# Kernel optimization log

Measured on AMD Instinct MI355X. Metric: run time of the kernel, lower is better.

The kernel has to match this reference:

```python
import jax, jax.numpy as jnp
import numpy as np

N_CHANNELS = 1024
N_HEADS = 16
BLOCK_SIZE = 2048
BATCH = 4
SEQ = 2048


def setup_inputs() -> dict:
    key = jax.random.key(0)
    k_x, k_wqkv, k_wproj = jax.random.split(key, 3)
    x = jax.random.normal(k_x, (BATCH, SEQ, N_CHANNELS), dtype=jnp.float32)
    # torch nn.Linear: y = x @ W.T + b, W shape [out, in], init normal(std=0.02)
    W_qkv = jax.random.normal(k_wqkv, (3 * N_CHANNELS, N_CHANNELS), dtype=jnp.float32) * 0.02
    b_qkv = jnp.zeros((3 * N_CHANNELS,), dtype=jnp.float32)
    W_proj = jax.random.normal(k_wproj, (N_CHANNELS, N_CHANNELS), dtype=jnp.float32) * 0.02
    b_proj = jnp.zeros((N_CHANNELS,), dtype=jnp.float32)
    return {"x": x, "W_qkv": W_qkv, "b_qkv": b_qkv, "W_proj": W_proj, "b_proj": b_proj}


def reference(x, W_qkv, b_qkv, W_proj, b_proj):
    bs, n, n_channels = x.shape
    n_heads = N_HEADS
    head_dim = n_channels // n_heads
    scale = head_dim ** (-0.5)

    qkv = x @ W_qkv.T + b_qkv                              # [b, n, 3C]
    qkv = qkv.reshape(bs, n, 3, n_heads, head_dim)
    q, k, v = qkv[:, :, 0], qkv[:, :, 1], qkv[:, :, 2]     # [b, n, h, d]

    logits = jnp.einsum('bthc,bshc->bhts', q, k) * scale   # [b, h, t, s]
    # causal mask: log(tril(ones)) = 0 below diagonal, -inf above
    causal = jnp.tril(jnp.ones((n, n), dtype=bool))
    logits = jnp.where(causal[None, None], logits, -jnp.inf)
    attn = jax.nn.softmax(logits, axis=-1)

    output = jnp.einsum('bhts,bshc->bthc', attn, v)        # [b, t, h, d]
    output = output.reshape(bs, n, n_channels)
    output = output @ W_proj.T + b_proj
    return output
```

## Files before the change

### kernel.cpp

```cpp
#include <hip/hip_runtime.h>
#include <hip/hip_bf16.h>
#include <stdint.h>

#define BATCH 4
#define SEQ   2048
#define NC    1024
#define NH    16
#define HD    64
#define NT    16

typedef __bf16 bf16x8 __attribute__((ext_vector_type(8)));
typedef __bf16 bf16x2 __attribute__((ext_vector_type(2)));
typedef float  f32x4  __attribute__((ext_vector_type(4)));
typedef float  f32x16 __attribute__((ext_vector_type(16)));

#define DEV __device__ __forceinline__

DEV unsigned short f2bf(float f) {
    union { float f; unsigned u; } v; v.f = f;
    unsigned r = (v.u + 0x7fffu + ((v.u >> 16) & 1u)) >> 16;
    return (unsigned short)r;
}

DEV float fast_exp2(float x) {
#if __has_builtin(__builtin_amdgcn_exp2f)
    return __builtin_amdgcn_exp2f(x);
#else
    return exp2f(x);
#endif
}

DEV void plane32_swap(uint32_t& a, uint32_t& b) {
#if __has_builtin(__builtin_amdgcn_permlane32_swap)
    auto r = __builtin_amdgcn_permlane32_swap(a, b, false, false);
    a = (uint32_t)r[0];
    b = (uint32_t)r[1];
#else
    uint32_t sa = __shfl_xor(a, 32), sb = __shfl_xor(b, 32);
    const bool hi = ((threadIdx.x & 63) >= 32);
    uint32_t na = hi ? sb : a;
    uint32_t nb = hi ? b : sa;
    a = na; b = nb;
#endif
}

#define GLDS16(gsrc, ldst)                                                           \
    __builtin_amdgcn_global_load_lds(                                                \
        (const __attribute__((address_space(1))) unsigned int*)(gsrc),               \
        (__attribute__((address_space(3))) unsigned int*)(ldst), 16, 0, 0)

__global__ void cvt_kernel(const float* __restrict__ in, unsigned short* __restrict__ out, int n4) {
    int i = blockIdx.x * 256 + threadIdx.x;
    if (i >= n4) return;
    float4 v = reinterpret_cast<const float4*>(in)[i];
    ushort4 o;
    o.x = f2bf(v.x); o.y = f2bf(v.y); o.z = f2bf(v.z); o.w = f2bf(v.w);
    reinterpret_cast<ushort4*>(out)[i] = o;
}

template <bool BF16_OUT>
__global__ __launch_bounds__(256, 2) void gemm_bt_kernel(
    const unsigned short* __restrict__ A,
    const unsigned short* __restrict__ W,
    const float* __restrict__ bias,
    void* __restrict__ Cout,
    int M, int N, int K, int scale_n, float scale)
{
    __shared__ __align__(16) char Alds[128 * 128];
    __shared__ __align__(16) char Blds[128 * 128];

    const int tid = threadIdx.x;
    const int w = tid >> 6, l = tid & 63, g = l >> 4, lr = l & 15;
    const int nt = N >> 7;
    const int cpx = gridDim.x >> 3;
    const int bid = (blockIdx.x & 7) * cpx + (blockIdx.x >> 3);
    const int mtile = bid / nt, ntile = bid % nt;
    const int m0 = mtile << 7, n0 = ntile << 7;
    const int wr = (w >> 1) << 6, wc = (w & 1) << 6;

    f32x4 acc[4][4] = {};

    for (int kt = 0; kt < K; kt += 64) {
        if (kt) __syncthreads();
#pragma unroll
        for (int i = 0; i < 4; ++i) {
            const int issue = (i << 2) + w;
            const int row = (issue << 3) + (l >> 3);
            const int chunk = (l & 7) ^ (row & 7);
            GLDS16((const char*)(A + (size_t)(m0 + row) * K + kt) + (chunk << 4),
                   Alds + (issue << 10));
        }
#pragma unroll
        for (int i = 0; i < 4; ++i) {
            const int issue = (i << 2) + w;
            const int row = (issue << 3) + (l >> 3);
            const int chunk = (l & 7) ^ (row & 7);
            GLDS16((const char*)(W + (size_t)(n0 + row) * K + kt) + (chunk << 4),
                   Blds + (issue << 10));
        }
        __syncthreads();

#pragma unroll
        for (int kb = 0; kb < 2; ++kb) {
            bf16x8 af[4], bfr[4];
#pragma unroll
            for (int mf = 0; mf < 4; ++mf) {
                const int row = wr + (mf << 4) + lr;
                const int chunk = ((kb << 2) + g) ^ (row & 7);
                af[mf] = *reinterpret_cast<const bf16x8*>(Alds + row * 128 + (chunk << 4));
            }
#pragma unroll
            for (int nf = 0; nf < 4; ++nf) {
                const int row = wc + (nf << 4) + lr;
                const int chunk = ((kb << 2) + g) ^ (row & 7);
                bfr[nf] = *reinterpret_cast<const bf16x8*>(Blds + row * 128 + (chunk << 4));
            }
#pragma unroll
            for (int mf = 0; mf < 4; ++mf)
#pragma unroll
                for (int nf = 0; nf < 4; ++nf)
                    acc[mf][nf] = __builtin_amdgcn_mfma_f32_16x16x32_bf16(
                        af[mf], bfr[nf], acc[mf][nf], 0, 0, 0);
        }
    }

#pragma unroll
    for (int mf = 0; mf < 4; ++mf) {
#pragma unroll
        for (int nf = 0; nf < 4; ++nf) {
            const int n = n0 + wc + (nf << 4) + lr;
            const float bscale = (n < scale_n) ? scale : 1.0f;
            const float bv = bias[n];
#pragma unroll
            for (int r = 0; r < 4; ++r) {
                const int m = m0 + wr + (mf << 4) + (g << 2) + r;
                float v2 = (acc[mf][nf][r] + bv) * bscale;
                if (BF16_OUT)
                    ((unsigned short*)Cout)[(size_t)m * N + n] = f2bf(v2);
                else
                    ((float*)Cout)[(size_t)m * N + n] = v2;
            }
        }
    }
}

__global__ __launch_bounds__(256, 4) void attn_kernel(
    const unsigned short* __restrict__ qkv,
    unsigned short* __restrict__ ctx)
{
    __shared__ __align__(16) char Klds[2][8192];
    __shared__ __align__(16) char Vt[2][8192];

    const int tid = threadIdx.x;
    const int w = tid >> 6, l = tid & 63, hi = l >> 5, lq = l & 31;
    const int bid = blockIdx.x;
    const int s = bid >> 8, u = (bid >> 6) & 3, r0 = bid & 63;
    const int v = (s & 1) ? 3 - u : u;
    const int qt = NT - 1 - (s << 2) - v;
    const int h = r0 >> 2, b = r0 & 3;
    const unsigned short* base = qkv + (size_t)b * SEQ * 3072 + h * 64;

    const int vkey0 = (tid >> 5) << 3;
    const int vd0   = (tid & 31) << 1;
    const int vcc0  = vkey0 >> 3;
    const unsigned short* vbase = base + 2048 + (size_t)vkey0 * 3072 + vd0;

    const int q0 = (qt << 7) + (w << 5);
    const int q = q0 + lq;
    const int ntiles = (qt + 1) << 1;

    bf16x8 qfr[4];
#pragma unroll
    for (int ds = 0; ds < 4; ++ds)
        qfr[ds] = *reinterpret_cast<const bf16x8*>(
            base + (size_t)q * 3072 + (ds << 4) + (hi << 3));

    f32x16 acc0 = {}, acc1 = {};
    float mrun = -INFINITY, lrun = 0.f;

    uint32_t vreg[8];

#pragma unroll
    for (int i = 0; i < 8; ++i)
        vreg[i] = *reinterpret_cast<const uint32_t*>(vbase + (size_t)i * 3072);
#pragma unroll
    for (int i = 0; i < 2; ++i) {
        const int issue = (i << 2) + w;
        const int row = (issue << 3) + (l >> 3);
        const int chunk = (l & 7) ^ (row & 7);
        GLDS16((const char*)(base + 1024 + (size_t)row * 3072) + (chunk << 4),
               Klds[0] + (issue << 10));
    }
    {
        uint4 a, bq;
        a.x = (vreg[0] & 0xffffu) | (vreg[1] << 16);
        a.y = (vreg[2] & 0xffffu) | (vreg[3] << 16);
        a.z = (vreg[4] & 0xffffu) | (vreg[5] << 16);
        a.w = (vreg[6] & 0xffffu) | (vreg[7] << 16);
        bq.x = (vreg[0] >> 16) | (vreg[1] & 0xffff0000u);
        bq.y = (vreg[2] >> 16) | (vreg[3] & 0xffff0000u);
        bq.z = (vreg[4] >> 16) | (vreg[5] & 0xffff0000u);
        bq.w = (vreg[6] >> 16) | (vreg[7] & 0xffff0000u);
        *reinterpret_cast<uint4*>(
            Vt[0] + vd0 * 128 + ((vcc0 ^ (vd0 & 7)) << 4)) = a;
        *reinterpret_cast<uint4*>(
            Vt[0] + (vd0 + 1) * 128 + ((vcc0 ^ ((vd0 + 1) & 7)) << 4)) = bq;
    }
    __syncthreads();

    for (int t = 0; t < ntiles; ++t) {
        const int cur = t & 1;
        const int kv0 = t << 6;
        const bool pf_ = (t + 1 < ntiles);

        if (pf_) {
            const int kv1 = kv0 + 64;
#pragma unroll
            for (int i = 0; i < 8; ++i)
                vreg[i] = *reinterpret_cast<const uint32_t*>(
                    vbase + (size_t)(kv1 + i) * 3072);
#pragma unroll
            for (int i = 0; i < 2; ++i) {
                const int issue = (i << 2) + w;
                const int row = (issue << 3) + (l >> 3);
                const int chunk = (l & 7) ^ (row & 7);
                GLDS16((const char*)(base + 1024 + (size_t)(kv1 + row) * 3072) + (chunk << 4),
                       Klds[cur ^ 1] + (issue << 10));
            }
        }

        if (kv0 <= q0 + 31) {
            const bool do1 = (kv0 + 32 <= q0 + 31);

            f32x16 st0 = {}, st1 = {};
            __builtin_amdgcn_s_setprio(1);
#pragma unroll
            for (int ds = 0; ds < 4; ++ds) {
                const int chunk = (((ds << 1) + hi) ^ (lq & 7)) << 4;
                bf16x8 k0 = *reinterpret_cast<const bf16x8*>(
                    Klds[cur] + lq * 128 + chunk);
                st0 = __builtin_amdgcn_mfma_f32_32x32x16_bf16(k0, qfr[ds], st0, 0, 0, 0);
            }
            if (do1) {
#pragma unroll
                for (int ds = 0; ds < 4; ++ds) {
                    const int chunk = (((ds << 1) + hi) ^ (lq & 7)) << 4;
                    bf16x8 k1 = *reinterpret_cast<const bf16x8*>(
                        Klds[cur] + (lq + 32) * 128 + chunk);
                    st1 = __builtin_amdgcn_mfma_f32_32x32x16_bf16(k1, qfr[ds], st1, 0, 0, 0);
                }
            }
            __builtin_amdgcn_s_setprio(0);

            if (kv0 + 31 > q0) {
#pragma unroll
                for (int r = 0; r < 16; ++r) {
                    const int key = kv0 + ((r & 3) + ((r >> 2) << 3) + (hi << 2));
                    if (key > q) st0[r] = -INFINITY;
                }
            }
            if (do1 && kv0 + 63 > q0) {
#pragma unroll
                for (int r = 0; r < 16; ++r) {
                    const int key = kv0 + 32 + ((r & 3) + ((r >> 2) << 3) + (hi << 2));
                    if (key > q) st1[r] = -INFINITY;
                }
            }

            float mt = st0[0];
#pragma unroll
            for (int r = 1; r < 16; ++r) mt = fmaxf(mt, st0[r]);
            if (do1) {
#pragma unroll
                for (int r = 0; r < 16; ++r) mt = fmaxf(mt, st1[r]);
            }
            mt = fmaxf(mt, __shfl_xor(mt, 32));
            if (__any(mt > mrun + 8.0f)) {
                const float mnew = fmaxf(mrun, mt);
                const float corr = fast_exp2(mrun - mnew);
                mrun = mnew;
                lrun *= corr;
#pragma unroll
                for (int r = 0; r < 16; ++r) { acc0[r] *= corr; acc1[r] *= corr; }
            }
            float rs = 0.f;
#pragma unroll
            for (int r = 0; r < 16; ++r) { st0[r] = fast_exp2(st0[r] - mrun); rs += st0[r]; }
            if (do1) {
#pragma unroll
                for (int r = 0; r < 16; ++r) { st1[r] = fast_exp2(st1[r] - mrun); rs += st1[r]; }
            }
            rs += __shfl_xor(rs, 32);
            lrun += rs;

            uint32_t pk0[8], pk1[8];
#pragma unroll
            for (int sp = 0; sp < 4; ++sp)
#pragma unroll
                for (int c = 0; c < 2; ++c) {
                    bf16x2 t0 = {(__bf16)st0[(sp << 2) + (c << 1)],
                                 (__bf16)st0[(sp << 2) + (c << 1) + 1]};
                    pk0[(sp << 1) + c] = __builtin_bit_cast(uint32_t, t0);
                }
            if (do1) {
#pragma unroll
                for (int sp = 0; sp < 4; ++sp)
#pragma unroll
                    for (int c = 0; c < 2; ++c) {
                        bf16x2 t1 = {(__bf16)st1[(sp << 2) + (c << 1)],
                                     (__bf16)st1[(sp << 2) + (c << 1) + 1]};
                        pk1[(sp << 1) + c] = __builtin_bit_cast(uint32_t, t1);
                    }
            }

            const int nkt = do1 ? 4 : 2;
            __builtin_amdgcn_s_setprio(1);
#pragma unroll
            for (int kt = 0; kt < 4; ++kt) {
                if (kt >= nkt) break;
                const int s0 = (kt & 1) << 1;
                uint32_t x0, x1, y0, y1;
                if (kt < 2) {
                    x0 = pk0[(s0 << 1) + 0]; x1 = pk0[(s0 << 1) + 1];
                    y0 = pk0[(s0 << 1) + 2]; y1 = pk0[(s0 << 1) + 3];
                } else {
                    x0 = pk1[(s0 << 1) + 0]; x1 = pk1[(s0 << 1) + 1];
                    y0 = pk1[(s0 << 1) + 2]; y1 = pk1[(s0 << 1) + 3];
                }
                plane32_swap(x0, y0);
                plane32_swap(x1, y1);
                union { uint32_t u[4]; bf16x8 v; } pf;
                pf.u[0] = x0; pf.u[1] = x1; pf.u[2] = y0; pf.u[3] = y1;

                const int cc = (kt << 1) + hi;
                const char* vt = Vt[cur];
                bf16x8 vf0 = *reinterpret_cast<const bf16x8*>(
                    vt + lq * 128 + ((cc ^ (lq & 7)) << 4));
                bf16x8 vf1 = *reinterpret_cast<const bf16x8*>(
                    vt + (lq + 32) * 128 + ((cc ^ (lq & 7)) << 4));
                acc0 = __builtin_amdgcn_mfma_f32_32x32x16_bf16(vf0, pf.v, acc0, 0, 0, 0);
                acc1 = __builtin_amdgcn_mfma_f32_32x32x16_bf16(vf1, pf.v, acc1, 0, 0, 0);
            }
            __builtin_amdgcn_s_setprio(0);
        }

        if (pf_) {
            uint4 a, bq;
            a.x = (vreg[0] & 0xffffu) | (vreg[1] << 16);
            a.y = (vreg[2] & 0xffffu) | (vreg[3] << 16);
            a.z = (vreg[4] & 0xffffu) | (vreg[5] << 16);
            a.w = (vreg[6] & 0xffffu) | (vreg[7] << 16);
            bq.x = (vreg[0] >> 16) | (vreg[1] & 0xffff0000u);
            bq.y = (vreg[2] >> 16) | (vreg[3] & 0xffff0000u);
            bq.z = (vreg[4] >> 16) | (vreg[5] & 0xffff0000u);
            bq.w = (vreg[6] >> 16) | (vreg[7] & 0xffff0000u);
            char* vt = Vt[cur ^ 1];
            *reinterpret_cast<uint4*>(
                vt + vd0 * 128 + ((vcc0 ^ (vd0 & 7)) << 4)) = a;
            *reinterpret_cast<uint4*>(
                vt + (vd0 + 1) * 128 + ((vcc0 ^ ((vd0 + 1) & 7)) << 4)) = bq;
            __syncthreads();
        }
    }

    {
        const float li = 1.0f / lrun;
        unsigned short* op = ctx + (size_t)(b * SEQ + q) * NC + h * HD;
#pragma unroll
        for (int r = 0; r < 16; ++r) {
            const int d = (r & 3) + ((r >> 2) << 3) + (hi << 2);
            op[d] = f2bf(acc0[r] * li);
            op[d + 32] = f2bf(acc1[r] * li);
        }
    }
}

extern "C" void kernel_launch(void* const* d_in, const int* in_sizes, int n_in,
                              void* d_out, int out_size, void* d_ws, size_t ws_size,
                              hipStream_t stream) {
    const float* x     = (const float*)d_in[0];
    const float* Wqkv  = (const float*)d_in[1];
    const float* bqkv  = (const float*)d_in[2];
    const float* Wproj = (const float*)d_in[3];
    const float* bproj = (const float*)d_in[4];
    float* out = (float*)d_out;

    const int M = BATCH * SEQ;
    unsigned short* ws = (unsigned short*)d_ws;
    unsigned short* xb     = ws;
    unsigned short* wqkvb  = xb + (size_t)M * NC;
    unsigned short* wprojb = wqkvb + (size_t)3 * NC * NC;
    unsigned short* qkvb   = wprojb + (size_t)NC * NC;
    unsigned short* ctxb   = qkvb + (size_t)M * 3 * NC;

    {
        int n4 = M * NC / 4;
        cvt_kernel<<<(n4 + 255) / 256, 256, 0, stream>>>(x, xb, n4);
    }
    {
        int n4 = 3 * NC * NC / 4;
        cvt_kernel<<<(n4 + 255) / 256, 256, 0, stream>>>(Wqkv, wqkvb, n4);
    }
    {
        int n4 = NC * NC / 4;
        cvt_kernel<<<(n4 + 255) / 256, 256, 0, stream>>>(Wproj, wprojb, n4);
    }

    gemm_bt_kernel<true><<<(M / 128) * (3 * NC / 128), 256, 0, stream>>>(
        xb, wqkvb, bqkv, qkvb, M, 3 * NC, NC, NC, 0.18033688011112042f);

    attn_kernel<<<NT * NH * BATCH, 256, 0, stream>>>(qkvb, ctxb);

    gemm_bt_kernel<false><<<(M / 128) * (NC / 128), 256, 0, stream>>>(
        ctxb, wprojb, bproj, out, M, NC, NC, 0, 1.0f);
}
```

Before: 160.2 us.

## Balance causal attention by pairing query tiles and splitting KV across thread groups

The attention kernel now launches 512-thread blocks made of two 256-thread groups. Each block owns a short query tile p and its mirror 15-p. Group 0 finishes tile p, then starts the first part of tile 15-p's KV range, while group 1 processes the rest of that range. The two partial softmax states (m, l, accumulators) are merged through LDS at the end, so every group runs exactly 17 KV tiles and the per-block imbalance of causal masking goes away. In exchange it adds a cross-group merge step, a larger LDS stage buffer, a 512-thread launch bound that tightens register limits, and half as many blocks. It also changes the V-tile swizzle expression.

Measured after the change: 189.3 us. +18.1%, slower.

```diff
diff --git a/kernel.cpp b/kernel.cpp
--- a/kernel.cpp
+++ b/kernel.cpp
@@ -144,30 +144,34 @@
     }
 }
 
-__global__ __launch_bounds__(256, 4) void attn_kernel(
+__global__ __launch_bounds__(512, 4) void attn_kernel(
     const unsigned short* __restrict__ qkv,
     unsigned short* __restrict__ ctx)
 {
-    __shared__ __align__(16) char Klds[2][8192];
-    __shared__ __align__(16) char Vt[2][8192];
+    __shared__ __align__(16) char Stage[2][2][2][8192];
 
     const int tid = threadIdx.x;
-    const int w = tid >> 6, l = tid & 63, hi = l >> 5, lq = l & 31;
+    const int g = tid >> 8;
+    const int tg = tid & 255;
+    const int w = tg >> 6;
+    const int l = tid & 63, hi = l >> 5, lq = l & 31;
     const int bid = blockIdx.x;
-    const int s = bid >> 8, u = (bid >> 6) & 3, r0 = bid & 63;
-    const int v = (s & 1) ? 3 - u : u;
-    const int qt = NT - 1 - (s << 2) - v;
-    const int h = r0 >> 2, b = r0 & 3;
+    const int p = bid >> 6;
+    const int hb = bid & 63;
+    const int h = hb >> 2, b = hb & 3;
+    const int P = NT - 1 - p;
     const unsigned short* base = qkv + (size_t)b * SEQ * 3072 + h * 64;
 
-    const int vkey0 = (tid >> 5) << 3;
-    const int vd0   = (tid & 31) << 1;
-    const int vcc0  = vkey0 >> 3;
+    const int switch_t = 2 * p + 2;
+    const int jB0 = 15 - 2 * p;
+
+    const int vkey0 = (tg >> 5) << 3;
+    const int vd0   = (tg & 31) << 1;
+    const int vphys = ((tg >> 5) ^ (tg & 7)) << 4;
     const unsigned short* vbase = base + 2048 + (size_t)vkey0 * 3072 + vd0;
 
-    const int q0 = (qt << 7) + (w << 5);
-    const int q = q0 + lq;
-    const int ntiles = (qt + 1) << 1;
+    int q0 = ((g == 0) ? p : P) * 128 + (w << 5);
+    int q = q0 + lq;
 
     bf16x8 qfr[4];
 #pragma unroll
@@ -177,21 +181,22 @@
 
     f32x16 acc0 = {}, acc1 = {};
     float mrun = -INFINITY, lrun = 0.f;
-
     uint32_t vreg[8];
 
-#pragma unroll
-    for (int i = 0; i < 8; ++i)
-        vreg[i] = *reinterpret_cast<const uint32_t*>(vbase + (size_t)i * 3072);
-#pragma unroll
-    for (int i = 0; i < 2; ++i) {
-        const int issue = (i << 2) + w;
-        const int row = (issue << 3) + (l >> 3);
-        const int chunk = (l & 7) ^ (row & 7);
-        GLDS16((const char*)(base + 1024 + (size_t)row * 3072) + (chunk << 4),
-               Klds[0] + (issue << 10));
-    }
     {
+        const int j0 = (g == 0) ? 0 : jB0;
+#pragma unroll
+        for (int i = 0; i < 8; ++i)
+            vreg[i] = *reinterpret_cast<const uint32_t*>(
+                vbase + (size_t)((j0 << 6) + i) * 3072);
+#pragma unroll
+        for (int i = 0; i < 2; ++i) {
+            const int issue = (i << 2) + w;
+            const int row = (issue << 3) + (l >> 3);
+            const int chunk = (l & 7) ^ (row & 7);
+            GLDS16((const char*)(base + 1024 + (size_t)((j0 << 6) + row) * 3072) + (chunk << 4),
+                   &Stage[g][0][0][0] + (issue << 10));
+        }
         uint4 a, bq;
         a.x = (vreg[0] & 0xffffu) | (vreg[1] << 16);
         a.y = (vreg[2] & 0xffffu) | (vreg[3] << 16);
@@ -201,52 +206,73 @@
         bq.y = (vreg[2] >> 16) | (vreg[3] & 0xffff0000u);
         bq.z = (vreg[4] >> 16) | (vreg[5] & 0xffff0000u);
         bq.w = (vreg[6] >> 16) | (vreg[7] & 0xffff0000u);
-        *reinterpret_cast<uint4*>(
-            Vt[0] + vd0 * 128 + ((vcc0 ^ (vd0 & 7)) << 4)) = a;
-        *reinterpret_cast<uint4*>(
-            Vt[0] + (vd0 + 1) * 128 + ((vcc0 ^ ((vd0 + 1) & 7)) << 4)) = bq;
+        char* vt = &Stage[g][0][1][0];
+        *reinterpret_cast<uint4*>(vt + vd0 * 128 + vphys) = a;
+        *reinterpret_cast<uint4*>(vt + (vd0 + 1) * 128 + vphys) = bq;
     }
     __syncthreads();
 
-    for (int t = 0; t < ntiles; ++t) {
+    for (int t = 0; t < 17; ++t) {
         const int cur = t & 1;
-        const int kv0 = t << 6;
-        const bool pf_ = (t + 1 < ntiles);
+        const int jc = (g == 0) ? ((t < switch_t) ? t : t - switch_t) : (jB0 + t);
+        const int kv0 = jc << 6;
+        const bool pf_ = (t + 1 < 17);
 
         if (pf_) {
-            const int kv1 = kv0 + 64;
+            const int jn = (g == 0) ? ((t + 1 < switch_t) ? t + 1 : t + 1 - switch_t)
+                                    : (jB0 + t + 1);
 #pragma unroll
             for (int i = 0; i < 8; ++i)
                 vreg[i] = *reinterpret_cast<const uint32_t*>(
-                    vbase + (size_t)(kv1 + i) * 3072);
+                    vbase + (size_t)((jn << 6) + i) * 3072);
 #pragma unroll
             for (int i = 0; i < 2; ++i) {
                 const int issue = (i << 2) + w;
                 const int row = (issue << 3) + (l >> 3);
                 const int chunk = (l & 7) ^ (row & 7);
-                GLDS16((const char*)(base + 1024 + (size_t)(kv1 + row) * 3072) + (chunk << 4),
-                       Klds[cur ^ 1] + (issue << 10));
-            }
+                GLDS16((const char*)(base + 1024 + (size_t)((jn << 6) + row) * 3072) + (chunk << 4),
+                       &Stage[g][cur ^ 1][0][0] + (issue << 10));
+            }
+        }
+
+        if (g == 0 && t == switch_t) {
+            const float li = 1.0f / lrun;
+            unsigned short* op = ctx + (size_t)(b * SEQ + q) * NC + h * HD;
+#pragma unroll
+            for (int r = 0; r < 16; ++r) {
+                const int d = (r & 3) + ((r >> 2) << 3) + (hi << 2);
+                op[d] = f2bf(acc0[r] * li);
+                op[d + 32] = f2bf(acc1[r] * li);
+            }
+            q0 = P * 128 + (w << 5);
+            q = q0 + lq;
+#pragma unroll
+            for (int ds = 0; ds < 4; ++ds)
+                qfr[ds] = *reinterpret_cast<const bf16x8*>(
+                    base + (size_t)q * 3072 + (ds << 4) + (hi << 3));
+#pragma unroll
+            for (int r = 0; r < 16; ++r) { acc0[r] = 0.f; acc1[r] = 0.f; }
+            mrun = -INFINITY; lrun = 0.f;
         }
 
         if (kv0 <= q0 + 31) {
             const bool do1 = (kv0 + 32 <= q0 + 31);
+            const char* Kl = &Stage[g][cur][0][0];
+            const char* Vl = &Stage[g][cur][1][0];
 
             f32x16 st0 = {}, st1 = {};
             __builtin_amdgcn_s_setprio(1);
 #pragma unroll
             for (int ds = 0; ds < 4; ++ds) {
                 const int chunk = (((ds << 1) + hi) ^ (lq & 7)) << 4;
-                bf16x8 k0 = *reinterpret_cast<const bf16x8*>(
-                    Klds[cur] + lq * 128 + chunk);
+                bf16x8 k0 = *reinterpret_cast<const bf16x8*>(Kl + lq * 128 + chunk);
                 st0 = __builtin_amdgcn_mfma_f32_32x32x16_bf16(k0, qfr[ds], st0, 0, 0, 0);
             }
             if (do1) {
 #pragma unroll
                 for (int ds = 0; ds < 4; ++ds) {
                     const int chunk = (((ds << 1) + hi) ^ (lq & 7)) << 4;
-                    bf16x8 k1 = *reinterpret_cast<const bf16x8*>(
-                        Klds[cur] + (lq + 32) * 128 + chunk);
+                    bf16x8 k1 = *reinterpret_cast<const bf16x8*>(Kl + (lq + 32) * 128 + chunk);
                     st1 = __builtin_amdgcn_mfma_f32_32x32x16_bf16(k1, qfr[ds], st1, 0, 0, 0);
                 }
             }
@@ -314,6 +340,7 @@
             }
 
             const int nkt = do1 ? 4 : 2;
+            const int fch = (lq >> 1) & 7;
             __builtin_amdgcn_s_setprio(1);
 #pragma unroll
             for (int kt = 0; kt < 4; ++kt) {
@@ -333,11 +360,10 @@
                 pf.u[0] = x0; pf.u[1] = x1; pf.u[2] = y0; pf.u[3] = y1;
 
                 const int cc = (kt << 1) + hi;
-                const char* vt = Vt[cur];
                 bf16x8 vf0 = *reinterpret_cast<const bf16x8*>(
-                    vt + lq * 128 + ((cc ^ (lq & 7)) << 4));
+                    Vl + lq * 128 + ((cc ^ fch) << 4));
                 bf16x8 vf1 = *reinterpret_cast<const bf16x8*>(
-                    vt + (lq + 32) * 128 + ((cc ^ (lq & 7)) << 4));
+                    Vl + (lq + 32) * 128 + ((cc ^ fch) << 4));
                 acc0 = __builtin_amdgcn_mfma_f32_32x32x16_bf16(vf0, pf.v, acc0, 0, 0, 0);
                 acc1 = __builtin_amdgcn_mfma_f32_32x32x16_bf16(vf1, pf.v, acc1, 0, 0, 0);
             }
@@ -354,23 +380,58 @@
             bq.y = (vreg[2] >> 16) | (vreg[3] & 0xffff0000u);
             bq.z = (vreg[4] >> 16) | (vreg[5] & 0xffff0000u);
             bq.w = (vreg[6] >> 16) | (vreg[7] & 0xffff0000u);
-            char* vt = Vt[cur ^ 1];
-            *reinterpret_cast<uint4*>(
-                vt + vd0 * 128 + ((vcc0 ^ (vd0 & 7)) << 4)) = a;
-            *reinterpret_cast<uint4*>(
-                vt + (vd0 + 1) * 128 + ((vcc0 ^ ((vd0 + 1) & 7)) << 4)) = bq;
+            char* vt = &Stage[g][cur ^ 1][1][0];
+            *reinterpret_cast<uint4*>(vt + vd0 * 128 + vphys) = a;
+            *reinterpret_cast<uint4*>(vt + (vd0 + 1) * 128 + vphys) = bq;
             __syncthreads();
         }
     }
 
-    {
-        const float li = 1.0f / lrun;
+    __syncthreads();
+    if (g == 0) {
+        float* OA = (float*)&Stage[0][0][0][0];
+        const int L = (w << 6) + l;
+        char* lb = (char*)OA + L * 128;
+#pragma unroll
+        for (int c = 0; c < 4; ++c) {
+            f32x4 t4 = {acc0[(c << 2)], acc0[(c << 2) + 1], acc0[(c << 2) + 2], acc0[(c << 2) + 3]};
+            *reinterpret_cast<f32x4*>(lb + ((c ^ (L & 7)) << 4)) = t4;
+        }
+#pragma unroll
+        for (int c = 4; c < 8; ++c) {
+            const int r0 = (c - 4) << 2;
+            f32x4 t4 = {acc1[r0], acc1[r0 + 1], acc1[r0 + 2], acc1[r0 + 3]};
+            *reinterpret_cast<f32x4*>(lb + ((c ^ (L & 7)) << 4)) = t4;
+        }
+        float* ml = (float*)&Stage[1][0][0][0];
+        if (hi == 0) {
+            ml[(((w << 5) + lq) << 1) + 0] = mrun;
+            ml[(((w << 5) + lq) << 1) + 1] = lrun;
+        }
+    }
+    __syncthreads();
+    if (g == 1) {
+        const float* OA = (const float*)&Stage[0][0][0][0];
+        const float* ml = (const float*)&Stage[1][0][0][0];
+        const int L = (w << 6) + l;
+        const char* lb = (const char*)OA + L * 128;
+        f32x4 oa[8];
+#pragma unroll
+        for (int c = 0; c < 8; ++c)
+            oa[c] = *reinterpret_cast<const f32x4*>(lb + ((c ^ (L & 7)) << 4));
+        const float mA = ml[(((w << 5) + lq) << 1) + 0];
+        const float lA = ml[(((w << 5) + lq) << 1) + 1];
+        const float m2 = fmaxf(mA, mrun);
+        float fa = fast_exp2(mA - m2);
+        float fb = fast_exp2(mrun - m2);
+        const float inv = 1.0f / (fa * lA + fb * lrun);
+        fa *= inv; fb *= inv;
         unsigned short* op = ctx + (size_t)(b * SEQ + q) * NC + h * HD;
 #pragma unroll
         for (int r = 0; r < 16; ++r) {
             const int d = (r & 3) + ((r >> 2) << 3) + (hi << 2);
-            op[d] = f2bf(acc0[r] * li);
-            op[d + 32] = f2bf(acc1[r] * li);
+            op[d]      = f2bf(fa * oa[r >> 2][r & 3]       + fb * acc0[r]);
+            op[d + 32] = f2bf(fa * oa[4 + (r >> 2)][r & 3] + fb * acc1[r]);
         }
     }
 }
@@ -409,7 +470,7 @@
     gemm_bt_kernel<true><<<(M / 128) * (3 * NC / 128), 256, 0, stream>>>(
         xb, wqkvb, bqkv, qkvb, M, 3 * NC, NC, NC, 0.18033688011112042f);
 
-    attn_kernel<<<NT * NH * BATCH, 256, 0, stream>>>(qkvb, ctxb);
+    attn_kernel<<<8 * NH * BATCH, 512, 0, stream>>>(qkvb, ctxb);
 
     gemm_bt_kernel<false><<<(M / 128) * (NC / 128), 256, 0, stream>>>(
         ctxb, wprojb, bproj, out, M, NC, NC, 0, 1.0f);
```

## Make attention kernel persistent with atomic ticket work queue over causal tiles

Applied to the files above, without the earlier changes.

Turns the attention kernel into a persistent kernel. Each block repeatedly takes a work item from a global atomic ticket, ordered longest causal query tile first, until the queue is empty. The ticket is reset by the first conversion kernel, and the grid is fixed at 1280 blocks with launch bounds raised to 5 blocks per SM. The aim is better dynamic load balancing of the uneven causal workloads, in exchange for atomic and extra barrier overhead per item and higher register pressure from the occupancy hint. The setprio hints around the MFMA sections are also removed.

After: 631.0 us. 294% more time.

```diff
diff --git a/kernel.cpp b/kernel.cpp
--- a/kernel.cpp
+++ b/kernel.cpp
@@ -8,6 +8,7 @@
 #define NH    16
 #define HD    64
 #define NT    16
+#define NITEMS (NT * NH * BATCH)
 
 typedef __bf16 bf16x8 __attribute__((ext_vector_type(8)));
 typedef __bf16 bf16x2 __attribute__((ext_vector_type(2)));
@@ -49,7 +50,9 @@
         (const __attribute__((address_space(1))) unsigned int*)(gsrc),               \
         (__attribute__((address_space(3))) unsigned int*)(ldst), 16, 0, 0)
 
-__global__ void cvt_kernel(const float* __restrict__ in, unsigned short* __restrict__ out, int n4) {
+__global__ void cvt_kernel(const float* __restrict__ in, unsigned short* __restrict__ out,
+                           int n4, unsigned int* ticket) {
+    if (ticket && blockIdx.x == 0 && threadIdx.x == 0) *ticket = 0;
     int i = blockIdx.x * 256 + threadIdx.x;
     if (i >= n4) return;
     float4 v = reinterpret_cast<const float4*>(in)[i];
@@ -144,207 +147,64 @@
     }
 }
 
-__global__ __launch_bounds__(256, 4) void attn_kernel(
+__global__ __launch_bounds__(256, 5) void attn_kernel(
     const unsigned short* __restrict__ qkv,
-    unsigned short* __restrict__ ctx)
+    unsigned short* __restrict__ ctx,
+    unsigned int* __restrict__ ticket)
 {
     __shared__ __align__(16) char Klds[2][8192];
     __shared__ __align__(16) char Vt[2][8192];
 
     const int tid = threadIdx.x;
     const int w = tid >> 6, l = tid & 63, hi = l >> 5, lq = l & 31;
-    const int bid = blockIdx.x;
-    const int s = bid >> 8, u = (bid >> 6) & 3, r0 = bid & 63;
-    const int v = (s & 1) ? 3 - u : u;
-    const int qt = NT - 1 - (s << 2) - v;
-    const int h = r0 >> 2, b = r0 & 3;
-    const unsigned short* base = qkv + (size_t)b * SEQ * 3072 + h * 64;
 
     const int vkey0 = (tid >> 5) << 3;
     const int vd0   = (tid & 31) << 1;
-    const int vcc0  = vkey0 >> 3;
-    const unsigned short* vbase = base + 2048 + (size_t)vkey0 * 3072 + vd0;
-
-    const int q0 = (qt << 7) + (w << 5);
-    const int q = q0 + lq;
-    const int ntiles = (qt + 1) << 1;
-
-    bf16x8 qfr[4];
-#pragma unroll
-    for (int ds = 0; ds < 4; ++ds)
-        qfr[ds] = *reinterpret_cast<const bf16x8*>(
-            base + (size_t)q * 3072 + (ds << 4) + (hi << 3));
-
-    f32x16 acc0 = {}, acc1 = {};
-    float mrun = -INFINITY, lrun = 0.f;
-
-    uint32_t vreg[8];
-
-#pragma unroll
-    for (int i = 0; i < 8; ++i)
-        vreg[i] = *reinterpret_cast<const uint32_t*>(vbase + (size_t)i * 3072);
-#pragma unroll
-    for (int i = 0; i < 2; ++i) {
-        const int issue = (i << 2) + w;
-        const int row = (issue << 3) + (l >> 3);
-        const int chunk = (l & 7) ^ (row & 7);
-        GLDS16((const char*)(base + 1024 + (size_t)row * 3072) + (chunk << 4),
-               Klds[0] + (issue << 10));
-    }
-    {
-        uint4 a, bq;
-        a.x = (vreg[0] & 0xffffu) | (vreg[1] << 16);
-        a.y = (vreg[2] & 0xffffu) | (vreg[3] << 16);
-        a.z = (vreg[4] & 0xffffu) | (vreg[5] << 16);
-        a.w = (vreg[6] & 0xffffu) | (vreg[7] << 16);
-        bq.x = (vreg[0] >> 16) | (vreg[1] & 0xffff0000u);
-        bq.y = (vreg[2] >> 16) | (vreg[3] & 0xffff0000u);
-        bq.z = (vreg[4] >> 16) | (vreg[5] & 0xffff0000u);
-        bq.w = (vreg[6] >> 16) | (vreg[7] & 0xffff0000u);
-        *reinterpret_cast<uint4*>(
-            Vt[0] + vd0 * 128 + ((vcc0 ^ (vd0 & 7)) << 4)) = a;
-        *reinterpret_cast<uint4*>(
-            Vt[0] + (vd0 + 1) * 128 + ((vcc0 ^ ((vd0 + 1) & 7)) << 4)) = bq;
-    }
-    __syncthreads();
-
-    for (int t = 0; t < ntiles; ++t) {
-        const int cur = t & 1;
-        const int kv0 = t << 6;
-        const bool pf_ = (t + 1 < ntiles);
-
-        if (pf_) {
-            const int kv1 = kv0 + 64;
-#pragma unroll
-            for (int i = 0; i < 8; ++i)
-                vreg[i] = *reinterpret_cast<const uint32_t*>(
-                    vbase + (size_t)(kv1 + i) * 3072);
-#pragma unroll
-            for (int i = 0; i < 2; ++i) {
-                const int issue = (i << 2) + w;
-                const int row = (issue << 3) + (l >> 3);
-                const int chunk = (l & 7) ^ (row & 7);
-                GLDS16((const char*)(base + 1024 + (size_t)(kv1 + row) * 3072) + (chunk << 4),
-                       Klds[cur ^ 1] + (issue << 10));
-            }
-        }
-
-        if (kv0 <= q0 + 31) {
-            const bool do1 = (kv0 + 32 <= q0 + 31);
-
-            f32x16 st0 = {}, st1 = {};
-            __builtin_amdgcn_s_setprio(1);
-#pragma unroll
-            for (int ds = 0; ds < 4; ++ds) {
-                const int chunk = (((ds << 1) + hi) ^ (lq & 7)) << 4;
-                bf16x8 k0 = *reinterpret_cast<const bf16x8*>(
-                    Klds[cur] + lq * 128 + chunk);
-                st0 = __builtin_amdgcn_mfma_f32_32x32x16_bf16(k0, qfr[ds], st0, 0, 0, 0);
-            }
-            if (do1) {
-#pragma unroll
-                for (int ds = 0; ds < 4; ++ds) {
-                    const int chunk = (((ds << 1) + hi) ^ (lq & 7)) << 4;
-                    bf16x8 k1 = *reinterpret_cast<const bf16x8*>(
-                        Klds[cur] + (lq + 32) * 128 + chunk);
-                    st1 = __builtin_amdgcn_mfma_f32_32x32x16_bf16(k1, qfr[ds], st1, 0, 0, 0);
-                }
-            }
-            __builtin_amdgcn_s_setprio(0);
-
-            if (kv0 + 31 > q0) {
-#pragma unroll
-                for (int r = 0; r < 16; ++r) {
-                    const int key = kv0 + ((r & 3) + ((r >> 2) << 3) + (hi << 2));
-                    if (key > q) st0[r] = -INFINITY;
-                }
-            }
-            if (do1 && kv0 + 63 > q0) {
-#pragma unroll
-                for (int r = 0; r < 16; ++r) {
-                    const int key = kv0 + 32 + ((r & 3) + ((r >> 2) << 3) + (hi << 2));
-                    if (key > q) st1[r] = -INFINITY;
-                }
-            }
-
-            float mt = st0[0];
-#pragma unroll
-            for (int r = 1; r < 16; ++r) mt = fmaxf(mt, st0[r]);
-            if (do1) {
-#pragma unroll
-                for (int r = 0; r < 16; ++r) mt = fmaxf(mt, st1[r]);
-            }
-            mt = fmaxf(mt, __shfl_xor(mt, 32));
-            if (__any(mt > mrun + 8.0f)) {
-                const float mnew = fmaxf(mrun, mt);
-                const float corr = fast_exp2(mrun - mnew);
-                mrun = mnew;
-                lrun *= corr;
-#pragma unroll
-                for (int r = 0; r < 16; ++r) { acc0[r] *= corr; acc1[r] *= corr; }
-            }
-            float rs = 0.f;
-#pragma unroll
-            for (int r = 0; r < 16; ++r) { st0[r] = fast_exp2(st0[r] - mrun); rs += st0[r]; }
-            if (do1) {
-#pragma unroll
-                for (int r = 0; r < 16; ++r) { st1[r] = fast_exp2(st1[r] - mrun); rs += st1[r]; }
-            }
-            rs += __shfl_xor(rs, 32);
-            lrun += rs;
-
-            uint32_t pk0[8], pk1[8];
-#pragma unroll
-            for (int sp = 0; sp < 4; ++sp)
-#pragma unroll
-                for (int c = 0; c < 2; ++c) {
-                    bf16x2 t0 = {(__bf16)st0[(sp << 2) + (c << 1)],
-                                 (__bf16)st0[(sp << 2) + (c << 1) + 1]};
-                    pk0[(sp << 1) + c] = __builtin_bit_cast(uint32_t, t0);
-                }
-            if (do1) {
-#pragma unroll
-                for (int sp = 0; sp < 4; ++sp)
-#pragma unroll
-                    for (int c = 0; c < 2; ++c) {
-                        bf16x2 t1 = {(__bf16)st1[(sp << 2) + (c << 1)],
-                                     (__bf16)st1[(sp << 2) + (c << 1) + 1]};
-                        pk1[(sp << 1) + c] = __builtin_bit_cast(uint32_t, t1);
-                    }
-            }
-
-            const int nkt = do1 ? 4 : 2;
-            __builtin_amdgcn_s_setprio(1);
-#pragma unroll
-            for (int kt = 0; kt < 4; ++kt) {
-                if (kt >= nkt) break;
-                const int s0 = (kt & 1) << 1;
-                uint32_t x0, x1, y0, y1;
-                if (kt < 2) {
-                    x0 = pk0[(s0 << 1) + 0]; x1 = pk0[(s0 << 1) + 1];
-                    y0 = pk0[(s0 << 1) + 2]; y1 = pk0[(s0 << 1) + 3];
-                } else {
-                    x0 = pk1[(s0 << 1) + 0]; x1 = pk1[(s0 << 1) + 1];
-                    y0 = pk1[(s0 << 1) + 2]; y1 = pk1[(s0 << 1) + 3];
-                }
-                plane32_swap(x0, y0);
-                plane32_swap(x1, y1);
-                union { uint32_t u[4]; bf16x8 v; } pf;
-                pf.u[0] = x0; pf.u[1] = x1; pf.u[2] = y0; pf.u[3] = y1;
-
-                const int cc = (kt << 1) + hi;
-                const char* vt = Vt[cur];
-                bf16x8 vf0 = *reinterpret_cast<const bf16x8*>(
-                    vt + lq * 128 + ((cc ^ (lq & 7)) << 4));
-                bf16x8 vf1 = *reinterpret_cast<const bf16x8*>(
-                    vt + (lq + 32) * 128 + ((cc ^ (lq & 7)) << 4));
-                acc0 = __builtin_amdgcn_mfma_f32_32x32x16_bf16(vf0, pf.v, acc0, 0, 0, 0);
-                acc1 = __builtin_amdgcn_mfma_f32_32x32x16_bf16(vf1, pf.v, acc1, 0, 0, 0);
-            }
-            __builtin_amdgcn_s_setprio(0);
-        }
-
-        if (pf_) {
+    const int vcc0  = tid >> 5;
+    const int vph1  = (vcc0 ^ (vd0 & 7)) << 4;
+    const int vph2  = (vcc0 ^ ((vd0 + 1) & 7)) << 4;
+
+    volatile int* sitem = (volatile int*)&Klds[0][0];
+
+    for (;;) {
+        __syncthreads();
+        if (tid == 0) *sitem = (int)atomicAdd(ticket, 1u);
+        __syncthreads();
+        const int it = *sitem;
+        __syncthreads();
+        if (it >= NITEMS) return;
+
+        const int qt = NT - 1 - (it >> 6);
+        const int h = (it >> 2) & 15, b = it & 3;
+        const unsigned short* base = qkv + (size_t)b * SEQ * 3072 + h * 64;
+        const unsigned short* vbase = base + 2048 + (size_t)vkey0 * 3072 + vd0;
+
+        const int q0 = (qt << 7) + (w << 5);
+        const int q = q0 + lq;
+        const int ntiles = (qt + 1) << 1;
+
+        bf16x8 qfr[4];
+#pragma unroll
+        for (int ds = 0; ds < 4; ++ds)
+            qfr[ds] = *reinterpret_cast<const bf16x8*>(
+                base + (size_t)q * 3072 + (ds << 4) + (hi << 3));
+
+        f32x16 acc0 = {}, acc1 = {};
+        float mrun = -INFINITY, lrun = 0.f;
+        uint32_t vreg[8];
+
+#pragma unroll
+        for (int i = 0; i < 8; ++i)
+            vreg[i] = *reinterpret_cast<const uint32_t*>(vbase + (size_t)i * 3072);
+#pragma unroll
+        for (int i = 0; i < 2; ++i) {
+            const int issue = (i << 2) + w;
+            const int row = (issue << 3) + (l >> 3);
+            const int chunk = (l & 7) ^ (row & 7);
+            GLDS16((const char*)(base + 1024 + (size_t)row * 3072) + (chunk << 4),
+                   &Klds[0][0] + (issue << 10));
+        }
+        {
             uint4 a, bq;
             a.x = (vreg[0] & 0xffffu) | (vreg[1] << 16);
             a.y = (vreg[2] & 0xffffu) | (vreg[3] << 16);
@@ -354,23 +214,169 @@
             bq.y = (vreg[2] >> 16) | (vreg[3] & 0xffff0000u);
             bq.z = (vreg[4] >> 16) | (vreg[5] & 0xffff0000u);
             bq.w = (vreg[6] >> 16) | (vreg[7] & 0xffff0000u);
-            char* vt = Vt[cur ^ 1];
-            *reinterpret_cast<uint4*>(
-                vt + vd0 * 128 + ((vcc0 ^ (vd0 & 7)) << 4)) = a;
-            *reinterpret_cast<uint4*>(
-                vt + (vd0 + 1) * 128 + ((vcc0 ^ ((vd0 + 1) & 7)) << 4)) = bq;
-            __syncthreads();
-        }
-    }
-
-    {
-        const float li = 1.0f / lrun;
-        unsigned short* op = ctx + (size_t)(b * SEQ + q) * NC + h * HD;
-#pragma unroll
-        for (int r = 0; r < 16; ++r) {
-            const int d = (r & 3) + ((r >> 2) << 3) + (hi << 2);
-            op[d] = f2bf(acc0[r] * li);
-            op[d + 32] = f2bf(acc1[r] * li);
+            *reinterpret_cast<uint4*>(&Vt[0][0] + vd0 * 128 + vph1) = a;
+            *reinterpret_cast<uint4*>(&Vt[0][0] + (vd0 + 1) * 128 + vph2) = bq;
+        }
+        __syncthreads();
+
+        for (int t = 0; t < ntiles; ++t) {
+            const int cur = t & 1;
+            const int kv0 = t << 6;
+            const bool pf_ = (t + 1 < ntiles);
+
+            if (pf_) {
+                const int kv1 = kv0 + 64;
+#pragma unroll
+                for (int i = 0; i < 8; ++i)
+                    vreg[i] = *reinterpret_cast<const uint32_t*>(
+                        vbase + (size_t)(kv1 + i) * 3072);
+#pragma unroll
+                for (int i = 0; i < 2; ++i) {
+                    const int issue = (i << 2) + w;
+                    const int row = (issue << 3) + (l >> 3);
+                    const int chunk = (l & 7) ^ (row & 7);
+                    GLDS16((const char*)(base + 1024 + (size_t)(kv1 + row) * 3072) + (chunk << 4),
+                           &Klds[cur ^ 1][0] + (issue << 10));
+                }
+            }
+
+            if (kv0 <= q0 + 31) {
+                const bool do1 = (kv0 + 32 <= q0 + 31);
+                const char* Kl = &Klds[cur][0];
+                const char* Vl = &Vt[cur][0];
+
+                f32x16 st0 = {}, st1 = {};
+#pragma unroll
+                for (int ds = 0; ds < 4; ++ds) {
+                    const int chunk = (((ds << 1) + hi) ^ (lq & 7)) << 4;
+                    bf16x8 k0 = *reinterpret_cast<const bf16x8*>(Kl + lq * 128 + chunk);
+                    st0 = __builtin_amdgcn_mfma_f32_32x32x16_bf16(k0, qfr[ds], st0, 0, 0, 0);
+                }
+                if (do1) {
+#pragma unroll
+                    for (int ds = 0; ds < 4; ++ds) {
+                        const int chunk = (((ds << 1) + hi) ^ (lq & 7)) << 4;
+                        bf16x8 k1 = *reinterpret_cast<const bf16x8*>(Kl + (lq + 32) * 128 + chunk);
+                        st1 = __builtin_amdgcn_mfma_f32_32x32x16_bf16(k1, qfr[ds], st1, 0, 0, 0);
+                    }
+                }
+
+                if (kv0 + 31 > q0) {
+#pragma unroll
+                    for (int r = 0; r < 16; ++r) {
+                        const int key = kv0 + ((r & 3) + ((r >> 2) << 3) + (hi << 2));
+                        if (key > q) st0[r] = -INFINITY;
+                    }
+                }
+                if (do1 && kv0 + 63 > q0) {
+#pragma unroll
+                    for (int r = 0; r < 16; ++r) {
+                        const int key = kv0 + 32 + ((r & 3) + ((r >> 2) << 3) + (hi << 2));
+                        if (key > q) st1[r] = -INFINITY;
+                    }
+                }
+
+                float mt = st0[0];
+#pragma unroll
+                for (int r = 1; r < 16; ++r) mt = fmaxf(mt, st0[r]);
+                if (do1) {
+#pragma unroll
+                    for (int r = 0; r < 16; ++r) mt = fmaxf(mt, st1[r]);
+                }
+                mt = fmaxf(mt, __shfl_xor(mt, 32));
+                if (__any(mt > mrun + 8.0f)) {
+                    const float mnew = fmaxf(mrun, mt);
+                    const float corr = fast_exp2(mrun - mnew);
+                    mrun = mnew;
+                    lrun *= corr;
+#pragma unroll
+                    for (int r = 0; r < 16; ++r) { acc0[r] *= corr; acc1[r] *= corr; }
+                }
+                float rs = 0.f;
+#pragma unroll
+                for (int r = 0; r < 16; ++r) { st0[r] = fast_exp2(st0[r] - mrun); rs += st0[r]; }
+                if (do1) {
+#pragma unroll
+                    for (int r = 0; r < 16; ++r) { st1[r] = fast_exp2(st1[r] - mrun); rs += st1[r]; }
+                }
+                rs += __shfl_xor(rs, 32);
+                lrun += rs;
+
+                uint32_t pk0[8], pk1[8];
+#pragma unroll
+                for (int sp = 0; sp < 4; ++sp)
+#pragma unroll
+                    for (int c = 0; c < 2; ++c) {
+                        bf16x2 t0 = {(__bf16)st0[(sp << 2) + (c << 1)],
+                                     (__bf16)st0[(sp << 2) + (c << 1) + 1]};
+                        pk0[(sp << 1) + c] = __builtin_bit_cast(uint32_t, t0);
+                    }
+                if (do1) {
+#pragma unroll
+                    for (int sp = 0; sp < 4; ++sp)
+#pragma unroll
+                        for (int c = 0; c < 2; ++c) {
+                            bf16x2 t1 = {(__bf16)st1[(sp << 2) + (c << 1)],
+                                         (__bf16)st1[(sp << 2) + (c << 1) + 1]};
+                            pk1[(sp << 1) + c] = __builtin_bit_cast(uint32_t, t1);
+                        }
+                }
+
+                const int nkt = do1 ? 4 : 2;
+                const int fch = lq & 7;
+#pragma unroll
+                for (int kt = 0; kt < 4; ++kt) {
+                    if (kt >= nkt) break;
+                    const int s0 = (kt & 1) << 1;
+                    uint32_t x0, x1, y0, y1;
+                    if (kt < 2) {
+                        x0 = pk0[(s0 << 1) + 0]; x1 = pk0[(s0 << 1) + 1];
+                        y0 = pk0[(s0 << 1) + 2]; y1 = pk0[(s0 << 1) + 3];
+                    } else {
+                        x0 = pk1[(s0 << 1) + 0]; x1 = pk1[(s0 << 1) + 1];
+                        y0 = pk1[(s0 << 1) + 2]; y1 = pk1[(s0 << 1) + 3];
+                    }
+                    plane32_swap(x0, y0);
+                    plane32_swap(x1, y1);
+                    union { uint32_t u[4]; bf16x8 v; } pf;
+                    pf.u[0] = x0; pf.u[1] = x1; pf.u[2] = y0; pf.u[3] = y1;
+
+                    const int cc = (kt << 1) + hi;
+                    bf16x8 vf0 = *reinterpret_cast<const bf16x8*>(
+                        Vl + lq * 128 + ((cc ^ fch) << 4));
+                    bf16x8 vf1 = *reinterpret_cast<const bf16x8*>(
+                        Vl + (lq + 32) * 128 + ((cc ^ fch) << 4));
+                    acc0 = __builtin_amdgcn_mfma_f32_32x32x16_bf16(vf0, pf.v, acc0, 0, 0, 0);
+                    acc1 = __builtin_amdgcn_mfma_f32_32x32x16_bf16(vf1, pf.v, acc1, 0, 0, 0);
+                }
+            }
+
+            if (pf_) {
+                uint4 a, bq;
+                a.x = (vreg[0] & 0xffffu) | (vreg[1] << 16);
+                a.y = (vreg[2] & 0xffffu) | (vreg[3] << 16);
+                a.z = (vreg[4] & 0xffffu) | (vreg[5] << 16);
+                a.w = (vreg[6] & 0xffffu) | (vreg[7] << 16);
+                bq.x = (vreg[0] >> 16) | (vreg[1] & 0xffff0000u);
+                bq.y = (vreg[2] >> 16) | (vreg[3] & 0xffff0000u);
+                bq.z = (vreg[4] >> 16) | (vreg[5] & 0xffff0000u);
+                bq.w = (vreg[6] >> 16) | (vreg[7] & 0xffff0000u);
+                char* vt = &Vt[cur ^ 1][0];
+                *reinterpret_cast<uint4*>(vt + vd0 * 128 + vph1) = a;
+                *reinterpret_cast<uint4*>(vt + (vd0 + 1) * 128 + vph2) = bq;
+                __syncthreads();
+            }
+        }
+
+        {
+            const float li = 1.0f / lrun;
+            unsigned short* op = ctx + (size_t)(b * SEQ + q) * NC + h * HD;
+#pragma unroll
+            for (int r = 0; r < 16; ++r) {
+                const int d = (r & 3) + ((r >> 2) << 3) + (hi << 2);
+                op[d] = f2bf(acc0[r] * li);
+                op[d + 32] = f2bf(acc1[r] * li);
+            }
         }
     }
 }
@@ -392,24 +398,25 @@
     unsigned short* wprojb = wqkvb + (size_t)3 * NC * NC;
     unsigned short* qkvb   = wprojb + (size_t)NC * NC;
     unsigned short* ctxb   = qkvb + (size_t)M * 3 * NC;
+    unsigned int* ticket   = (unsigned int*)(ctxb + (size_t)M * NC);
 
     {
         int n4 = M * NC / 4;
-        cvt_kernel<<<(n4 + 255) / 256, 256, 0, stream>>>(x, xb, n4);
+        cvt_kernel<<<(n4 + 255) / 256, 256, 0, stream>>>(x, xb, n4, ticket);
     }
     {
         int n4 = 3 * NC * NC / 4;
-        cvt_kernel<<<(n4 + 255) / 256, 256, 0, stream>>>(Wqkv, wqkvb, n4);
+        cvt_kernel<<<(n4 + 255) / 256, 256, 0, stream>>>(Wqkv, wqkvb, n4, nullptr);
     }
     {
         int n4 = NC * NC / 4;
-        cvt_kernel<<<(n4 + 255) / 256, 256, 0, stream>>>(Wproj, wprojb, n4);
+        cvt_kernel<<<(n4 + 255) / 256, 256, 0, stream>>>(Wproj, wprojb, n4, nullptr);
     }
 
     gemm_bt_kernel<true><<<(M / 128) * (3 * NC / 128), 256, 0, stream>>>(
         xb, wqkvb, bqkv, qkvb, M, 3 * NC, NC, NC, 0.18033688011112042f);
 
-    attn_kernel<<<NT * NH * BATCH, 256, 0, stream>>>(qkvb, ctxb);
+    attn_kernel<<<1280, 256, 0, stream>>>(qkvb, ctxb, ticket);
 
     gemm_bt_kernel<false><<<(M / 128) * (NC / 128), 256, 0, stream>>>(
         ctxb, wprojb, bproj, out, M, NC, NC, 0, 1.0f);
```
